# Optimization experiments

Measured on AMD Instinct MI355X. Metric: run time of the kernel, lower is better.

The kernel has to match this reference:

```python
import jax, jax.numpy as jnp
import numpy as np

NP_, NT_, NA_, NG_ = 50000, 200000, 20000, 500
ED, HID, H, C, L = 64, 64, 4, 16, 2
NEG_SLOPE = 0.2


def _edges(key, e, ns, nd):
    k1, k2 = jax.random.split(key)
    return jnp.stack([jax.random.randint(k1, (e,), 0, ns, dtype=jnp.int32),
                      jax.random.randint(k2, (e,), 0, nd, dtype=jnp.int32)])


def setup_inputs() -> dict:
    key = jax.random.key(0)
    ks = iter(jax.random.split(key, 64))
    nrm = lambda shp, s=0.1: (jax.random.normal(next(ks), shp, jnp.float32) * s)
    inp = {
        'playlist_x': nrm((NP_, 8), 1.0), 'track_x': nrm((NT_, 7), 1.0),
        'artist_x': nrm((NA_, 1), 1.0), 'genre_x': nrm((NG_, NG_), 1.0),
        'emb_playlist': nrm((NP_, ED)), 'emb_artist': nrm((NA_, ED)),
        'pf_W': nrm((8, ED)), 'pf_b': jnp.zeros((ED,)),
        'tf_W': nrm((7, ED)), 'tf_b': jnp.zeros((ED,)),
        'af_W': nrm((1, ED)), 'af_b': jnp.zeros((ED,)),
        'gf_W': nrm((NG_, ED)), 'gf_b': jnp.zeros((ED,)),
        'ip_W_playlist': nrm((2 * ED, HID)), 'ip_b_playlist': jnp.zeros((HID,)),
        'ip_W_track': nrm((ED, HID)), 'ip_b_track': jnp.zeros((HID,)),
        'ip_W_artist': nrm((2 * ED, HID)), 'ip_b_artist': jnp.zeros((HID,)),
        'ip_W_genre': nrm((ED, HID)), 'ip_b_genre': jnp.zeros((HID,)),
        # 8 relations x L layers, shared lin per relation (PyG GATConv with int in_channels)
        'gat_W': nrm((L, 8, HID, H * C)), 'gat_b': jnp.zeros((L, 8, H * C)),
        'gat_as': nrm((L, 8, H, C)), 'gat_ad': nrm((L, 8, H, C)),
        'ln_w': jnp.ones((L, HID)), 'ln_b': jnp.zeros((L, HID)),
        'op_W_playlist': nrm((HID, ED)), 'op_b_playlist': jnp.zeros((ED,)),
        'op_W_track': nrm((HID, ED)), 'op_b_track': jnp.zeros((ED,)),
        'op_W_artist': nrm((HID, ED)), 'op_b_artist': jnp.zeros((ED,)),
        'op_W_genre': nrm((HID, ED)), 'op_b_genre': jnp.zeros((ED,)),
        'playlist_idx': jnp.arange(NP_, dtype=jnp.int32),
        'artist_idx': jnp.arange(NA_, dtype=jnp.int32),
        'ei_contains': _edges(next(ks), 1000000, NP_, NT_),
        'ei_in_playlist': _edges(next(ks), 1000000, NT_, NP_),
        'ei_by': _edges(next(ks), 200000, NT_, NA_),
        'ei_created': _edges(next(ks), 200000, NA_, NT_),
        'ei_has_genre': _edges(next(ks), 600000, NT_, NG_),
        'ei_includes': _edges(next(ks), 600000, NG_, NT_),
        'ei_performs': _edges(next(ks), 60000, NA_, NG_),
        'ei_performed_by': _edges(next(ks), 60000, NG_, NA_),
    }
    return inp


def _gat(x_src, x_dst, ei, W, b, a_s, a_d, n_dst):
    # PyG GATConv: shared lin, edge softmax over dst, scatter-add aggregation
    hs = (x_src @ W).reshape(x_src.shape[0], H, C)
    hd = (x_dst @ W).reshape(x_dst.shape[0], H, C)
    es, ed = ei[0], ei[1]
    al_s = jnp.einsum('nhc,hc->nh', hs, a_s)  # [Ns,H]
    al_d = jnp.einsum('nhc,hc->nh', hd, a_d)  # [Nd,H]
    alpha = jax.nn.leaky_relu(al_s[es] + al_d[ed], NEG_SLOPE)  # [E,H]
    amax = jax.ops.segment_max(alpha, ed, num_segments=n_dst)
    amax = jnp.where(jnp.isfinite(amax), amax, 0.0)
    ex = jnp.exp(alpha - amax[ed])
    den = jax.ops.segment_sum(ex, ed, num_segments=n_dst)
    coef = ex / (den[ed] + 1e-16)
    msg = (hs[es] * coef[:, :, None]).reshape(es.shape[0], H * C)  # [E,H*C]
    return jax.ops.segment_sum(msg, ed, num_segments=n_dst) + b


def _ln(x, w, b):
    m = jnp.mean(x, -1, keepdims=True)
    v = jnp.mean((x - m) ** 2, -1, keepdims=True)
    return (x - m) * jax.lax.rsqrt(v + 1e-5) * w + b


def _forward(playlist_x, track_x, artist_x, genre_x, emb_playlist, emb_artist,
             pf_W, pf_b, tf_W, tf_b, af_W, af_b, gf_W, gf_b,
             ip_W_playlist, ip_b_playlist, ip_W_track, ip_b_track,
             ip_W_artist, ip_b_artist, ip_W_genre, ip_b_genre,
             gat_W, gat_b, gat_as, gat_ad, ln_w, ln_b,
             op_W_playlist, op_b_playlist, op_W_track, op_b_track,
             op_W_artist, op_b_artist, op_W_genre, op_b_genre,
             playlist_idx, artist_idx, ei_contains, ei_in_playlist, ei_by,
             ei_created, ei_has_genre, ei_includes, ei_performs, ei_performed_by):
    h_p = jnp.concatenate([emb_playlist[playlist_idx], playlist_x @ pf_W + pf_b], -1) @ ip_W_playlist + ip_b_playlist
    h_t = (track_x @ tf_W + tf_b) @ ip_W_track + ip_b_track
    h_a = jnp.concatenate([emb_artist[artist_idx], artist_x @ af_W + af_b], -1) @ ip_W_artist + ip_b_artist
    h_g = (genre_x @ gf_W + gf_b) @ ip_W_genre + ip_b_genre
    for i in range(L):
        pp, pt, pa, pg = h_p, h_t, h_a, h_g
        g = lambda r, xs, xd, ei, nd: _gat(xs, xd, ei, gat_W[i, r], gat_b[i, r], gat_as[i, r], gat_ad[i, r], nd)
        # relation index: 0 contains,1 in_playlist,2 by,3 created,4 has_genre,5 includes_track,6 performs_genre,7 performed_by
        nt = g(0, pp, pt, ei_contains, NT_) + g(3, pa, pt, ei_created, NT_) + g(5, pg, pt, ei_includes, NT_)
        np2 = g(1, pt, pp, ei_in_playlist, NP_)
        na = g(2, pt, pa, ei_by, NA_) + g(7, pg, pa, ei_performed_by, NA_)
        ng = g(4, pt, pg, ei_has_genre, NG_) + g(6, pa, pg, ei_performs, NG_)
        h_p, h_t, h_a, h_g = jax.nn.relu(np2), jax.nn.relu(nt), jax.nn.relu(na), jax.nn.relu(ng)
        if i > 0:  # residual only after first layer (matches `if i > 0`)
            h_p, h_t, h_a, h_g = h_p + pp, h_t + pt, h_a + pa, h_g + pg
        h_p, h_t, h_a, h_g = (_ln(v, ln_w[i], ln_b[i]) for v in (h_p, h_t, h_a, h_g))
    return jnp.concatenate([
        h_p @ op_W_playlist + op_b_playlist,
        h_t @ op_W_track + op_b_track,
        h_a @ op_W_artist + op_b_artist,
        h_g @ op_W_genre + op_b_genre], axis=0)  # [NP+NT+NA+NG, 64]


def reference(playlist_x, track_x, artist_x, genre_x, emb_playlist, emb_artist,
              pf_W, pf_b, tf_W, tf_b, af_W, af_b, gf_W, gf_b,
              ip_W_playlist, ip_b_playlist, ip_W_track, ip_b_track,
              ip_W_artist, ip_b_artist, ip_W_genre, ip_b_genre,
              gat_W, gat_b, gat_as, gat_ad, ln_w, ln_b,
              op_W_playlist, op_b_playlist, op_W_track, op_b_track,
              op_W_artist, op_b_artist, op_W_genre, op_b_genre,
              playlist_idx, artist_idx, ei_contains, ei_in_playlist, ei_by,
              ei_created, ei_has_genre, ei_includes, ei_performs, ei_performed_by):
    return _forward(playlist_x, track_x, artist_x, genre_x, emb_playlist, emb_artist,
                    pf_W, pf_b, tf_W, tf_b, af_W, af_b, gf_W, gf_b,
                    ip_W_playlist, ip_b_playlist, ip_W_track, ip_b_track,
                    ip_W_artist, ip_b_artist, ip_W_genre, ip_b_genre,
                    gat_W, gat_b, gat_as, gat_ad, ln_w, ln_b,
                    op_W_playlist, op_b_playlist, op_W_track, op_b_track,
                    op_W_artist, op_b_artist, op_W_genre, op_b_genre,
                    playlist_idx, artist_idx, ei_contains, ei_in_playlist, ei_by,
                    ei_created, ei_has_genre, ei_includes, ei_performs, ei_performed_by)
```

## Files before the change

kernel.cpp:

```cpp
#include <hip/hip_runtime.h>
#include <cstdint>

constexpr int NP=50000, NT=200000, NA=20000, NG=500;
constexpr int NTOT = NP+NT+NA+NG;
constexpr int RO_P=0, RO_T=NP, RO_A=NP+NT, RO_G=NP+NT+NA;
constexpr int E_TOT = 3720000;

constexpr int H_E [8] = {1000000,1000000,200000,200000,600000,600000,60000,60000};
constexpr int H_ES[9] = {0,1000000,2000000,2200000,2400000,3000000,3600000,3660000,3720000};
constexpr int H_NS[8] = {NP,NT,NT,NA,NT,NG,NA,NG};
constexpr int H_ND[8] = {NT,NP,NA,NT,NG,NT,NG,NA};
constexpr int H_SO[8] = {RO_P,RO_T,RO_T,RO_A,RO_T,RO_G,RO_A,RO_G};
constexpr int H_DO[8] = {RO_T,RO_P,RO_A,RO_T,RO_G,RO_T,RO_G,RO_A};
constexpr int H_RPO[8]= {0,200001,250002,270003,470004,470505,670506,671007};
constexpr int H_CO[8] = {0,200000,250000,270000,470000,470500,670500,671000};

__constant__ int c_E [8] = {1000000,1000000,200000,200000,600000,600000,60000,60000};
__constant__ int c_ES[9] = {0,1000000,2000000,2200000,2400000,3000000,3600000,3660000,3720000};
__constant__ int c_ND[8] = {200000,50000,20000,200000,500,200000,500,20000};
__constant__ int c_RPO[8]= {0,200001,250002,270003,470004,470505,670506,671007};
__constant__ int c_CO[8] = {0,200000,250000,270000,470000,470500,670500,671000};

__constant__ int sb_pref[9] = {0,196,245,265,461,462,658,659,679};
constexpr int SB_BLOCKS = 679;

constexpr int WSZ = 16384;
__constant__ int c_G [8] = {16,16,4,4,10,10,2,2};
__constant__ int c_CS[8] = {62500,62500,50000,50000,60000,60000,30000,30000};
__constant__ int c_NW[8] = {13,4,2,13,1,13,1,2};
__constant__ int gw_pref[9] = {0,208,272,280,332,342,472,474,478};
constexpr int GW_BLOCKS = 478;
__constant__ int c_C2[8] = {0,3200000,4000000,4080000,4880000,4885000,6885000,6886000};

constexpr int OWT=0;
constexpr int OBT=448;
constexpr int OWPX=512;
constexpr int OBP=1024;
constexpr int OAV=1088;
constexpr int OBA=1152;
constexpr int OBG=1216;
constexpr int OBAGG=1280;
constexpr int OWAS=1792;
constexpr int OWAD=5888;
constexpr int OWG=9984;

struct EiPtrs { const int* p[8]; };

__device__ __forceinline__ unsigned short f2bf(float f){
  unsigned u = __float_as_uint(f);
  u += 0x7FFF + ((u>>16)&1);
  return (unsigned short)(u>>16);
}
__device__ __forceinline__ float bf2f(unsigned short b){
  return __uint_as_float(((unsigned)b)<<16);
}

__global__ __launch_bounds__(256) void k_prep(
  const float* __restrict__ pf_W, const float* __restrict__ pf_b,
  const float* __restrict__ tf_W, const float* __restrict__ tf_b,
  const float* __restrict__ af_W, const float* __restrict__ af_b,
  const float* __restrict__ gf_W, const float* __restrict__ gf_b,
  const float* __restrict__ ipWp, const float* __restrict__ ipbp,
  const float* __restrict__ ipWt, const float* __restrict__ ipbt,
  const float* __restrict__ ipWa, const float* __restrict__ ipba,
  const float* __restrict__ ipWg, const float* __restrict__ ipbg,
  const float* __restrict__ gatW, const float* __restrict__ gatB,
  const float* __restrict__ gatAs, const float* __restrict__ gatAd,
  float* __restrict__ cb)
{
  int tid = blockIdx.x*256 + threadIdx.x;
  int STR = gridDim.x*256;
  for(int i=tid;i<7*64;i+=STR){ int j=i>>6,c=i&63; float s=0.f;
    for(int k=0;k<64;k++) s += tf_W[j*64+k]*ipWt[k*64+c];
    cb[OWT+i]=s; }
  for(int i=tid;i<64;i+=STR){ float s=ipbt[i];
    for(int k=0;k<64;k++) s += tf_b[k]*ipWt[k*64+i];
    cb[OBT+i]=s; }
  for(int i=tid;i<8*64;i+=STR){ int j=i>>6,c=i&63; float s=0.f;
    for(int k=0;k<64;k++) s += pf_W[j*64+k]*ipWp[(64+k)*64+c];
    cb[OWPX+i]=s; }
  for(int i=tid;i<64;i+=STR){ float s=ipbp[i];
    for(int k=0;k<64;k++) s += pf_b[k]*ipWp[(64+k)*64+i];
    cb[OBP+i]=s; }
  for(int i=tid;i<64;i+=STR){ float s=0.f;
    for(int k=0;k<64;k++) s += af_W[k]*ipWa[(64+k)*64+i];
    cb[OAV+i]=s; }
  for(int i=tid;i<64;i+=STR){ float s=ipba[i];
    for(int k=0;k<64;k++) s += af_b[k]*ipWa[(64+k)*64+i];
    cb[OBA+i]=s; }
  for(int i=tid;i<64;i+=STR){ float s=ipbg[i];
    for(int k=0;k<64;k++) s += gf_b[k]*ipWg[k*64+i];
    cb[OBG+i]=s; }
  for(int i=tid;i<512;i+=STR){ int l=i>>8, t=(i>>6)&3, c=i&63;
    const float* B = gatB + l*8*64; float s;
    if(t==0)      s = B[1*64+c];
    else if(t==1) s = B[0*64+c]+B[3*64+c]+B[5*64+c];
    else if(t==2) s = B[2*64+c]+B[7*64+c];
    else          s = B[4*64+c]+B[6*64+c];
    cb[OBAGG+i]=s; }
  for(int i=tid;i<2*8*64*4;i+=STR){ int h=i&3, k=(i>>2)&63, lr=i>>8;
    const float* as = gatAs + lr*64;
    cb[OWAS+i] = ((k>>4)==h) ? as[h*16 + (k&15)] : 0.f;
    const float* W  = gatW + (size_t)lr*4096;
    const float* ad = gatAd + lr*64 + h*16;
    float d=0.f;
    for(int c=0;c<16;c++){ d += W[k*64+h*16+c]*ad[c]; }
    cb[OWAD+i]=d; }
  for(int i=tid;i<512*64;i+=STR){ int g=i>>6,c=i&63; float s=0.f;
    if(g<500){ for(int k=0;k<64;k++) s += gf_W[g*64+k]*ipWg[k*64+c]; }
    cb[OWG+i]=s; }
}

#define MM_DECL  __shared__ float sX[64*65]; __shared__ float sW[64*68]; \
  int tid=threadIdx.x; int rt=(tid>>4)<<2, ct=(tid&15)<<2; float acc[4][4];

#define MM_LOOP() \
  _Pragma("unroll 8") \
  for(int k=0;k<64;k++){ \
    float4 wv = *(const float4*)&sW[k*68+ct]; \
    float x0=sX[(rt+0)*65+k], x1=sX[(rt+1)*65+k], x2=sX[(rt+2)*65+k], x3=sX[(rt+3)*65+k]; \
    acc[0][0]+=x0*wv.x; acc[0][1]+=x0*wv.y; acc[0][2]+=x0*wv.z; acc[0][3]+=x0*wv.w; \
    acc[1][0]+=x1*wv.x; acc[1][1]+=x1*wv.y; acc[1][2]+=x1*wv.z; acc[1][3]+=x1*wv.w; \
    acc[2][0]+=x2*wv.x; acc[2][1]+=x2*wv.y; acc[2][2]+=x2*wv.z; acc[2][3]+=x2*wv.w; \
    acc[3][0]+=x3*wv.x; acc[3][1]+=x3*wv.y; acc[3][2]+=x3*wv.z; acc[3][3]+=x3*wv.w; \
  }

template<bool ALS, bool B16>
__global__ __launch_bounds__(256) void k_mm64(const float* __restrict__ X, const float* __restrict__ W,
  const float* __restrict__ bias, float* __restrict__ Y, float* __restrict__ alsY,
  const float* __restrict__ was, int N)
{
  MM_DECL
  int row0 = blockIdx.x*64;
  for(int i=tid;i<4096;i+=256){
    int r=i>>6, k=i&63;
    sX[r*65+k] = (row0+r<N)? X[(size_t)(row0+r)*64+k] : 0.f;
    sW[r*68+k] = W[i];
  }
  __syncthreads();
  #pragma unroll
  for(int i=0;i<4;i++){ acc[i][0]=0.f;acc[i][1]=0.f;acc[i][2]=0.f;acc[i][3]=0.f; }
  MM_LOOP()
  float4 bv = make_float4(0.f,0.f,0.f,0.f);
  if(bias) bv = *(const float4*)&bias[ct];
  #pragma unroll
  for(int i=0;i<4;i++){
    int row=row0+rt+i;
    if(row<N){
      if(B16){
        ushort4 o;
        o.x=f2bf(acc[i][0]+bv.x); o.y=f2bf(acc[i][1]+bv.y);
        o.z=f2bf(acc[i][2]+bv.z); o.w=f2bf(acc[i][3]+bv.w);
        *(ushort4*)&((unsigned short*)Y)[(size_t)row*64+ct] = o;
      } else {
        *(float4*)&Y[(size_t)row*64+ct] =
          make_float4(acc[i][0]+bv.x, acc[i][1]+bv.y, acc[i][2]+bv.z, acc[i][3]+bv.w);
      }
    }
  }
  if(ALS){
    float4 w0 = *(const float4*)&was[(ct+0)*4];
    float4 w1 = *(const float4*)&was[(ct+1)*4];
    float4 w2 = *(const float4*)&was[(ct+2)*4];
    float4 w3 = *(const float4*)&was[(ct+3)*4];
    #pragma unroll
    for(int i=0;i<4;i++){
      float4 p;
      p.x = acc[i][0]*w0.x + acc[i][1]*w1.x + acc[i][2]*w2.x + acc[i][3]*w3.x;
      p.y = acc[i][0]*w0.y + acc[i][1]*w1.y + acc[i][2]*w2.y + acc[i][3]*w3.y;
      p.z = acc[i][0]*w0.z + acc[i][1]*w1.z + acc[i][2]*w2.z + acc[i][3]*w3.z;
      p.w = acc[i][0]*w0.w + acc[i][1]*w1.w + acc[i][2]*w2.w + acc[i][3]*w3.w;
      #pragma unroll
      for(int m=1;m<16;m<<=1){
        p.x+=__shfl_xor(p.x,m); p.y+=__shfl_xor(p.y,m);
        p.z+=__shfl_xor(p.z,m); p.w+=__shfl_xor(p.w,m);
      }
      int row=row0+rt+i;
      if((tid&15)==0 && row<N) *(float4*)&alsY[(size_t)row*4] = p;
    }
  }
}

constexpr int BP=(NP+63)/64, BT=(NT+63)/64, BA=(NA+63)/64;
__global__ __launch_bounds__(256) void k_init(
  const float* __restrict__ px, const float* __restrict__ tx, const float* __restrict__ ax,
  const float* __restrict__ embp, const float* __restrict__ emba,
  const int* __restrict__ pidx, const int* __restrict__ aidx,
  const float* __restrict__ ipWp, const float* __restrict__ ipWa,
  const float* __restrict__ cb, float* __restrict__ hout)
{
  MM_DECL
  __shared__ float sE[64*9];
  int bid = blockIdx.x;
  if(bid < BP){
    int row0 = bid*64;
    for(int i=tid;i<4096;i+=256){
      int r=i>>6,k=i&63; int row=row0+r;
      sX[r*65+k] = (row<NP)? embp[(size_t)pidx[row]*64+k] : 0.f;
      sW[r*68+k] = ipWp[i];
    }
    for(int i=tid;i<512;i+=256){ int r=i>>3,j=i&7; int row=row0+r;
      sE[r*9+j] = (row<NP)? px[(size_t)row*8+j] : 0.f; }
    __syncthreads();
    { float4 b = *(const float4*)&cb[OBP+ct];
      #pragma unroll
      for(int i=0;i<4;i++){ acc[i][0]=b.x;acc[i][1]=b.y;acc[i][2]=b.z;acc[i][3]=b.w; } }
    #pragma unroll
    for(int j=0;j<8;j++){
      float4 w = *(const float4*)&cb[OWPX + j*64 + ct];
      #pragma unroll
      for(int i=0;i<4;i++){ float xe = sE[(rt+i)*9+j];
        acc[i][0]+=xe*w.x; acc[i][1]+=xe*w.y; acc[i][2]+=xe*w.z; acc[i][3]+=xe*w.w; }
    }
    MM_LOOP()
    #pragma unroll
    for(int i=0;i<4;i++){ int row=row0+rt+i;
      if(row<NP) *(float4*)&hout[(size_t)(RO_P+row)*64+ct] =
        make_float4(acc[i][0],acc[i][1],acc[i][2],acc[i][3]); }
  } else if(bid < BP+BT){
    int row0 = (bid-BP)*64;
    for(int i=tid;i<512;i+=256){ int r=i>>3,j=i&7; int row=row0+r;
      sE[r*9+j] = (row<NT && j<7)? tx[(size_t)row*7+j] : 0.f; }
    __syncthreads();
    { float4 b = *(const float4*)&cb[OBT+ct];
      #pragma unroll
      for(int i=0;i<4;i++){ acc[i][0]=b.x;acc[i][1]=b.y;acc[i][2]=b.z;acc[i][3]=b.w; } }
    #pragma unroll
    for(int j=0;j<7;j++){
      float4 w = *(const float4*)&cb[OWT + j*64 + ct];
      #pragma unroll
      for(int i=0;i<4;i++){ float xe = sE[(rt+i)*9+j];
        acc[i][0]+=xe*w.x; acc[i][1]+=xe*w.y; acc[i][2]+=xe*w.z; acc[i][3]+=xe*w.w; }
    }
    #pragma unroll
    for(int i=0;i<4;i++){ int row=row0+rt+i;
      if(row<NT) *(float4*)&hout[(size_t)(RO_T+row)*64+ct] =
        make_float4(acc[i][0],acc[i][1],acc[i][2],acc[i][3]); }
  } else {
    int row0 = (bid-BP-BT)*64;
    for(int i=tid;i<4096;i+=256){
      int r=i>>6,k=i&63; int row=row0+r;
      sX[r*65+k] = (row<NA)? emba[(size_t)aidx[row]*64+k] : 0.f;
      sW[r*68+k] = ipWa[i];
    }
    for(int i=tid;i<64;i+=256){ int row=row0+i; sE[i] = (row<NA)? ax[row] : 0.f; }
    __syncthreads();
    #pragma unroll
    for(int i=0;i<4;i++){
      float4 b = *(const float4*)&cb[OBA+ct];
      float4 av = *(const float4*)&cb[OAV+ct];
      float xe = sE[rt+i];
      acc[i][0]=b.x+xe*av.x; acc[i][1]=b.y+xe*av.y; acc[i][2]=b.z+xe*av.z; acc[i][3]=b.w+xe*av.w;
    }
    MM_LOOP()
    #pragma unroll
    for(int i=0;i<4;i++){ int row=row0+rt+i;
      if(row<NA) *(float4*)&hout[(size_t)(RO_A+row)*64+ct] =
        make_float4(acc[i][0],acc[i][1],acc[i][2],acc[i][3]); }
  }
}

__global__ __launch_bounds__(256) void k_init_g(const float* __restrict__ gx,
  const float* __restrict__ cb, float* __restrict__ hout)
{
  int wid = (blockIdx.x<<2)|(threadIdx.x>>6);
  int lane = threadIdx.x&63;
  if(wid>=NG) return;
  float acc = cb[OBG+lane];
  const float* WG = cb+OWG;
  for(int kb=0;kb<512;kb+=64){
    int k = kb+lane;
    float xv = (k<500)? gx[(size_t)wid*500+k] : 0.f;
    for(int j=0;j<64;j++){
      float x = __shfl(xv, j);
      acc += x * WG[(size_t)(kb+j)*64+lane];
    }
  }
  hout[(size_t)(RO_G+wid)*64+lane] = acc;
}

__global__ __launch_bounds__(1024) void k_cnt2(EiPtrs ei, int* __restrict__ cnt2){
  __shared__ int wcnt[WSZ];
  int bid=blockIdx.x, tid=threadIdx.x;
  int r=0;
  #pragma unroll
  for(int q=1;q<8;q++) if(bid>=gw_pref[q]) r=q;
  int local = bid - gw_pref[r];
  int NW=c_NW[r];
  int g = local/NW, w = local-g*NW;
  int lo=w*WSZ, nd=c_ND[r], n=min(WSZ,nd-lo);
  for(int i=tid;i<n;i+=1024) wcnt[i]=0;
  __syncthreads();
  int E=c_E[r], CS=c_CS[r];
  int e0=g*CS, e1=min(e0+CS,E);
  const int* __restrict__ pd = ei.p[r]+E;
  for(int e=e0+tid;e<e1;e+=1024){
    int d = pd[e]-lo;
    if((unsigned)d < (unsigned)n) atomicAdd(&wcnt[d],1);
  }
  __syncthreads();
  int* c = cnt2 + c_C2[r] + g*nd + lo;
  for(int i=tid;i<n;i+=1024) c[i]=wcnt[i];
}

__global__ __launch_bounds__(1024) void k_scan1(const int* __restrict__ cnt2, int* __restrict__ bsum){
  int bid = blockIdx.x;
  int r=0;
  #pragma unroll
  for(int q=1;q<8;q++) if(bid>=sb_pref[q]) r=q;
  int lb = bid - sb_pref[r];
  int nd = c_ND[r];
  int idx = lb*1024 + threadIdx.x;
  int v = 0;
  if(idx<nd){
    int G=c_G[r]; int base=c_C2[r]+idx;
    for(int g=0;g<G;g++) v += cnt2[base+g*nd];
  }
  #pragma unroll
  for(int m=1;m<64;m<<=1) v += __shfl_xor(v,m);
  __shared__ int wsum[16];
  int lane = threadIdx.x&63, wid=threadIdx.x>>6;
  if(lane==0) wsum[wid]=v;
  __syncthreads();
  if(threadIdx.x==0){
    int s=0;
    #pragma unroll
    for(int w=0;w<16;w++) s+=wsum[w];
    bsum[bid]=s;
  }
}

__global__ __launch_bounds__(256) void k_scan2(int* __restrict__ bsum, int* __restrict__ rowptr){
  int r = blockIdx.x;
  int nb = sb_pref[r+1]-sb_pref[r];
  __shared__ int s[200];
  int tid=threadIdx.x;
  if(tid<nb) s[tid]=bsum[sb_pref[r]+tid];
  __syncthreads();
  if(tid==0){
    int run=0;
    for(int i=0;i<nb;i++){ int t=s[i]; s[i]=run; run+=t; }
    rowptr[c_RPO[r]+c_ND[r]] = run;
  }
  __syncthreads();
  if(tid<nb) bsum[sb_pref[r]+tid]=s[tid];
}

__global__ __launch_bounds__(1024) void k_scan3(const int* __restrict__ cnt2, const int* __restrict__ bsum,
  int* __restrict__ rowptr){
  int bid = blockIdx.x;
  int r=0;
  #pragma unroll
  for(int q=1;q<8;q++) if(bid>=sb_pref[q]) r=q;
  int lb = bid - sb_pref[r];
  int nd = c_ND[r];
  int tid = threadIdx.x;
  int idx = lb*1024 + tid;
  int v = 0;
  if(idx<nd){
    int G=c_G[r]; int base=c_C2[r]+idx;
    for(int g=0;g<G;g++) v += cnt2[base+g*nd];
  }
  __shared__ int s[1024];
  s[tid]=v;
  __syncthreads();
  #pragma unroll
  for(int off=1;off<1024;off<<=1){
    int t = (tid>=off)? s[tid-off] : 0;
    __syncthreads();
    s[tid]+=t;
    __syncthreads();
  }
  int ex = s[tid]-v + bsum[bid];
  if(idx<nd) rowptr[c_RPO[r]+idx]=ex;
}

__global__ __launch_bounds__(1024) void k_off2(const int* __restrict__ rowptr, int* __restrict__ cnt2){
  int bid = blockIdx.x;
  int r=0;
  #pragma unroll
  for(int q=1;q<8;q++) if(bid>=sb_pref[q]) r=q;
  int idx = (bid-sb_pref[r])*1024 + threadIdx.x;
  int nd = c_ND[r];
  if(idx<nd){
    int run = rowptr[c_RPO[r]+idx];
    int G=c_G[r]; int base=c_C2[r]+idx;
    for(int g=0;g<G;g++){
      int t = cnt2[base+g*nd];
      cnt2[base+g*nd] = run;
      run += t;
    }
  }
}

__global__ __launch_bounds__(1024) void k_scat2(EiPtrs ei, const int* __restrict__ off2,
  int* __restrict__ col){
  __shared__ int wcur[WSZ];
  int bid=blockIdx.x, tid=threadIdx.x;
  int r=0;
  #pragma unroll
  for(int q=1;q<8;q++) if(bid>=gw_pref[q]) r=q;
  int local = bid - gw_pref[r];
  int NW=c_NW[r];
  int g = local/NW, w = local-g*NW;
  int lo=w*WSZ, nd=c_ND[r], n=min(WSZ,nd-lo);
  const int* o = off2 + c_C2[r] + g*nd + lo;
  for(int i=tid;i<n;i+=1024) wcur[i]=o[i];
  __syncthreads();
  int E=c_E[r], CS=c_CS[r];
  int e0=g*CS, e1=min(e0+CS,E);
  const int* __restrict__ ps = ei.p[r];
  const int* __restrict__ pd = ps+E;
  int* cl = col + c_ES[r];
  for(int e=e0+tid;e<e1;e+=1024){
    int d = pd[e]-lo;
    if((unsigned)d < (unsigned)n){
      int pos = atomicAdd(&wcur[d],1);
      cl[pos] = ps[e];
    }
  }
}

template<bool FIRST>
__global__ __launch_bounds__(256) void k_agg(const int* __restrict__ rp, const int* __restrict__ col,
  const unsigned short* __restrict__ hs, const float* __restrict__ als,
  const float* __restrict__ Xd, const float* __restrict__ wad,
  float* __restrict__ out, int nd)
{
  int wid = (blockIdx.x<<2)|(threadIdx.x>>6);
  int lane = threadIdx.x&63;
  if(wid>=nd) return;
  float x = Xd[(size_t)wid*64+lane];
  float4 wv = *(const float4*)&wad[lane*4];
  float a0=x*wv.x, a1=x*wv.y, a2=x*wv.z, a3=x*wv.w;
  #pragma unroll
  for(int m=1;m<64;m<<=1){
    a0+=__shfl_xor(a0,m); a1+=__shfl_xor(a1,m); a2+=__shfl_xor(a2,m); a3+=__shfl_xor(a3,m);
  }
  int h = lane>>4;
  float adv = (h==0)?a0:(h==1)?a1:(h==2)?a2:a3;
  int start = rp[wid], end = rp[wid+1];
  float den=0.f, acc=0.f;
  int j = start;
  for(; j+4<=end; j+=4){
    int s0=col[j], s1=col[j+1], s2=col[j+2], s3=col[j+3];
    float A0=als[(size_t)s0*4+h], A1=als[(size_t)s1*4+h];
    float A2=als[(size_t)s2*4+h], A3=als[(size_t)s3*4+h];
    float h0=bf2f(hs[(size_t)s0*64+lane]), h1=bf2f(hs[(size_t)s1*64+lane]);
    float h2=bf2f(hs[(size_t)s2*64+lane]), h3=bf2f(hs[(size_t)s3*64+lane]);
    float v0=A0+adv; v0=fmaxf(v0,0.2f*v0); float e0=__expf(v0);
    float v1=A1+adv; v1=fmaxf(v1,0.2f*v1); float e1=__expf(v1);
    float v2=A2+adv; v2=fmaxf(v2,0.2f*v2); float e2=__expf(v2);
    float v3=A3+adv; v3=fmaxf(v3,0.2f*v3); float e3=__expf(v3);
    den+=e0; acc+=e0*h0;
    den+=e1; acc+=e1*h1;
    den+=e2; acc+=e2*h2;
    den+=e3; acc+=e3*h3;
  }
  for(; j<end; j++){
    int s = col[j];
    float ah = als[(size_t)s*4+h] + adv;
    ah = fmaxf(ah, 0.2f*ah);
    float e = __expf(ah);
    den += e;
    acc += e*bf2f(hs[(size_t)s*64+lane]);
  }
  float r = acc/(den+1e-16f);
  if(FIRST) out[(size_t)wid*64+lane] = r;
  else      out[(size_t)wid*64+lane] += r;
}

template<bool FIRST>
__global__ __launch_bounds__(1024) void k_agg_blk(const int* __restrict__ rp, const int* __restrict__ col,
  const unsigned short* __restrict__ hs, const float* __restrict__ als,
  const float* __restrict__ Xd, const float* __restrict__ wad,
  float* __restrict__ out, int nd)
{
  int d = blockIdx.x;
  if(d>=nd) return;
  int tid=threadIdx.x, lane=tid&63, wid=tid>>6;
  __shared__ float sden[16*4];
  __shared__ float sacc[16][64];
  float x = Xd[(size_t)d*64+lane];
  float4 wv = *(const float4*)&wad[lane*4];
  float a0=x*wv.x, a1=x*wv.y, a2=x*wv.z, a3=x*wv.w;
  #pragma unroll
  for(int m=1;m<64;m<<=1){
    a0+=__shfl_xor(a0,m); a1+=__shfl_xor(a1,m); a2+=__shfl_xor(a2,m); a3+=__shfl_xor(a3,m);
  }
  int h = lane>>4;
  float adv = (h==0)?a0:(h==1)?a1:(h==2)?a2:a3;
  int start = rp[d], end = rp[d+1];
  float den=0.f, acc=0.f;
  int j = start+wid;
  for(; j+48<end; j+=64){
    int s0=col[j], s1=col[j+16], s2=col[j+32], s3=col[j+48];
    float A0=als[(size_t)s0*4+h], A1=als[(size_t)s1*4+h];
    float A2=als[(size_t)s2*4+h], A3=als[(size_t)s3*4+h];
    float h0=bf2f(hs[(size_t)s0*64+lane]), h1=bf2f(hs[(size_t)s1*64+lane]);
    float h2=bf2f(hs[(size_t)s2*64+lane]), h3=bf2f(hs[(size_t)s3*64+lane]);
    float v0=A0+adv; v0=fmaxf(v0,0.2f*v0); float e0=__expf(v0);
    float v1=A1+adv; v1=fmaxf(v1,0.2f*v1); float e1=__expf(v1);
    float v2=A2+adv; v2=fmaxf(v2,0.2f*v2); float e2=__expf(v2);
    float v3=A3+adv; v3=fmaxf(v3,0.2f*v3); float e3=__expf(v3);
    den+=e0; acc+=e0*h0;
    den+=e1; acc+=e1*h1;
    den+=e2; acc+=e2*h2;
    den+=e3; acc+=e3*h3;
  }
  for(; j<end; j+=16){
    int s = col[j];
    float ah = als[(size_t)s*4+h] + adv;
    ah = fmaxf(ah, 0.2f*ah);
    float e = __expf(ah);
    den += e;
    acc += e*bf2f(hs[(size_t)s*64+lane]);
  }
  if((lane&15)==0) sden[wid*4+h]=den;
  sacc[wid][lane]=acc;
  __syncthreads();
  if(tid<64){
    float s=0.f, dt=0.f;
    #pragma unroll
    for(int w=0;w<16;w++){ s+=sacc[w][tid]; dt+=sden[w*4+(tid>>4)]; }
    float r = s/(dt+1e-16f);
    if(FIRST) out[(size_t)d*64+tid] = r;
    else      out[(size_t)d*64+tid] += r;
  }
}

__global__ __launch_bounds__(256) void k_post(float* __restrict__ hnew, const float* __restrict__ hold,
  const float* __restrict__ bagg, const float* __restrict__ lnw, const float* __restrict__ lnb, int layer)
{
  int wid = (blockIdx.x<<2)|(threadIdx.x>>6);
  int lane = threadIdx.x&63;
  if(wid>=NTOT) return;
  int t = (wid<RO_T)?0 : (wid<RO_A)?1 : (wid<RO_G)?2 : 3;
  size_t idx = (size_t)wid*64+lane;
  float v = hnew[idx] + bagg[t*64+lane];
  v = fmaxf(v, 0.f);
  if(layer) v += hold[idx];
  float s = v;
  #pragma unroll
  for(int m=1;m<64;m<<=1) s += __shfl_xor(s,m);
  float mu = s*(1.f/64.f);
  float d = v-mu;
  float q = d*d;
  #pragma unroll
  for(int m=1;m<64;m<<=1) q += __shfl_xor(q,m);
  float var = q*(1.f/64.f);
  hnew[idx] = d*rsqrtf(var+1e-5f)*lnw[lane] + lnb[lane];
}

extern "C" void kernel_launch(void* const* d_in, const int* in_sizes, int n_in,
                              void* d_out, int out_size, void* d_ws, size_t ws_size,
                              hipStream_t stream)
{
  const float* playlist_x=(const float*)d_in[0];
  const float* track_x   =(const float*)d_in[1];
  const float* artist_x  =(const float*)d_in[2];
  const float* genre_x   =(const float*)d_in[3];
  const float* embp=(const float*)d_in[4];
  const float* emba=(const float*)d_in[5];
  const float* pf_W=(const float*)d_in[6];  const float* pf_b=(const float*)d_in[7];
  const float* tf_W=(const float*)d_in[8];  const float* tf_b=(const float*)d_in[9];
  const float* af_W=(const float*)d_in[10]; const float* af_b=(const float*)d_in[11];
  const float* gf_W=(const float*)d_in[12]; const float* gf_b=(const float*)d_in[13];
  const float* ipWp=(const float*)d_in[14]; const float* ipbp=(const float*)d_in[15];
  const float* ipWt=(const float*)d_in[16]; const float* ipbt=(const float*)d_in[17];
  const float* ipWa=(const float*)d_in[18]; const float* ipba=(const float*)d_in[19];
  const float* ipWg=(const float*)d_in[20]; const float* ipbg=(const float*)d_in[21];
  const float* gatW=(const float*)d_in[22]; const float* gatB=(const float*)d_in[23];
  const float* gatAs=(const float*)d_in[24];const float* gatAd=(const float*)d_in[25];
  const float* lnw=(const float*)d_in[26];  const float* lnb=(const float*)d_in[27];
  const float* opWp=(const float*)d_in[28]; const float* opbp=(const float*)d_in[29];
  const float* opWt=(const float*)d_in[30]; const float* opbt=(const float*)d_in[31];
  const float* opWa=(const float*)d_in[32]; const float* opba=(const float*)d_in[33];
  const float* opWg=(const float*)d_in[34]; const float* opbg=(const float*)d_in[35];
  const int* pidx=(const int*)d_in[36];
  const int* aidx=(const int*)d_in[37];
  EiPtrs ei;
  for(int r=0;r<8;r++) ei.p[r]=(const int*)d_in[38+r];

  char* ws=(char*)d_ws;
  float* cb = (float*)ws;
  size_t o_hB  = 256*1024;
  float* hB = (float*)(ws+o_hB);
  size_t o_hs  = o_hB  + (size_t)NTOT*64*4;
  unsigned short* hs16 = (unsigned short*)(ws+o_hs);
  size_t o_als = o_hs  + (size_t)NT*64*2;
  float* als=(float*)(ws+o_als);
  size_t o_rp  = o_als + (size_t)NT*4*4;
  int* rowptr=(int*)(ws+o_rp);
  size_t o_col = o_rp  + 691008*4;
  int* col=(int*)(ws+o_col);
  int* cnt2=(int*)(ws+o_hs);
  int* bsum=cnt2+6926000;
  float* hA=(float*)d_out;

  k_prep<<<128,256,0,stream>>>(pf_W,pf_b,tf_W,tf_b,af_W,af_b,gf_W,gf_b,
      ipWp,ipbp,ipWt,ipbt,ipWa,ipba,ipWg,ipbg,gatW,gatB,gatAs,gatAd,cb);
  k_init<<<BP+BT+BA,256,0,stream>>>(playlist_x,track_x,artist_x,embp,emba,pidx,aidx,ipWp,ipWa,cb,hA);
  k_init_g<<<(NG+3)/4,256,0,stream>>>(genre_x,cb,hA);

  k_cnt2<<<GW_BLOCKS,1024,0,stream>>>(ei,cnt2);
  k_scan1<<<SB_BLOCKS,1024,0,stream>>>(cnt2,bsum);
  k_scan2<<<8,256,0,stream>>>(bsum,rowptr);
  k_scan3<<<SB_BLOCKS,1024,0,stream>>>(cnt2,bsum,rowptr);
  k_off2<<<SB_BLOCKS,1024,0,stream>>>(rowptr,cnt2);
  k_scat2<<<GW_BLOCKS,1024,0,stream>>>(ei,cnt2,col);

  for(int l=0;l<2;l++){
    float* hcur = l? hB : hA;
    float* hnew = l? hA : hB;
    for(int r=0;r<8;r++){
      int Ns=H_NS[r], Nd=H_ND[r];
      const float* Xs = hcur + (size_t)H_SO[r]*64;
      const float* Xd = hcur + (size_t)H_DO[r]*64;
      const float* W  = gatW + (size_t)(l*8+r)*4096;
      const float* was = cb+OWAS+(size_t)(l*8+r)*256;
      const float* wad = cb+OWAD+(size_t)(l*8+r)*256;
      float* outp = hnew + (size_t)H_DO[r]*64;
      bool first = (r==0)||(r==1)||(r==2)||(r==4);
      k_mm64<true,true><<<(Ns+63)/64,256,0,stream>>>(Xs,W,nullptr,(float*)hs16,als,was,Ns);
      if(r==4 || r==6){
        if(first) k_agg_blk<true ><<<Nd,1024,0,stream>>>(rowptr+H_RPO[r], col+H_ES[r], hs16, als, Xd, wad, outp, Nd);
        else      k_agg_blk<false><<<Nd,1024,0,stream>>>(rowptr+H_RPO[r], col+H_ES[r], hs16, als, Xd, wad, outp, Nd);
      } else {
        if(first) k_agg<true ><<<(Nd+3)/4,256,0,stream>>>(rowptr+H_RPO[r], col+H_ES[r], hs16, als, Xd, wad, outp, Nd);
        else      k_agg<false><<<(Nd+3)/4,256,0,stream>>>(rowptr+H_RPO[r], col+H_ES[r], hs16, als, Xd, wad, outp, Nd);
      }
    }
    k_post<<<(NTOT+3)/4,256,0,stream>>>(hnew, hcur, cb+OBAGG+l*256, lnw+l*64, lnb+l*64, l);
  }
  k_mm64<false,false><<<(NP+63)/64,256,0,stream>>>(hA+(size_t)RO_P*64, opWp, opbp, hA+(size_t)RO_P*64, nullptr, nullptr, NP);
  k_mm64<false,false><<<(NT+63)/64,256,0,stream>>>(hA+(size_t)RO_T*64, opWt, opbt, hA+(size_t)RO_T*64, nullptr, nullptr, NT);
  k_mm64<false,false><<<(NA+63)/64,256,0,stream>>>(hA+(size_t)RO_A*64, opWa, opba, hA+(size_t)RO_A*64, nullptr, nullptr, NA);
  k_mm64<false,false><<<(NG+63)/64,256,0,stream>>>(hA+(size_t)RO_G*64, opWg, opbg, hA+(size_t)RO_G*64, nullptr, nullptr, NG);
}
```

Before: 1.429 ms.

## Batch all relation projections and fuse per-destination GAT aggregation with layer norm

Replaces the per-relation loop of projection and aggregation launches with one batched projection kernel over all eight relations, writing into a combined workspace, and one per-node kernel. That kernel aggregates every incoming relation for a node, then applies bias, ReLU, residual and LayerNorm in place. This removes many kernel launches, the read-modify-write accumulation across relations, and the separate post pass. It needs a larger workspace and falls back to the old path when the workspace is too small. It also drops the block-per-node path for the genre relations, so each of the 500 genre nodes is handled by a single wavefront over thousands of edges, which risks a long tail.

```diff
diff --git a/kernel.cpp b/kernel.cpp
--- a/kernel.cpp
+++ b/kernel.cpp
@@ -20,6 +20,12 @@
 __constant__ int c_ND[8] = {200000,50000,20000,200000,500,200000,500,20000};
 __constant__ int c_RPO[8]= {0,200001,250002,270003,470004,470505,670506,671007};
 __constant__ int c_CO[8] = {0,200000,250000,270000,470000,470500,670500,671000};
+__constant__ int c_NS[8] = {50000,200000,200000,20000,200000,500,20000,500};
+__constant__ int c_SO[8] = {0,50000,50000,250000,50000,270000,250000,270000};
+__constant__ int c_DO[8] = {50000,0,250000,50000,270000,50000,270000,250000};
+__constant__ int c_RSO[8]= {0,50000,250000,450000,470000,670000,670500,690500};
+__constant__ int c_mmp[9]= {0,782,3907,7032,7345,10470,10478,10791,10799};
+constexpr int MM_ALL_BLOCKS = 10799;
 
 __constant__ int sb_pref[9] = {0,196,245,265,461,462,658,659,679};
 constexpr int SB_BLOCKS = 679;
@@ -181,6 +187,138 @@
   }
 }
 
+__global__ __launch_bounds__(256) void k_mm64_all(const float* __restrict__ hcur,
+  const float* __restrict__ gatW, const float* __restrict__ cb,
+  unsigned short* __restrict__ hs_all, float* __restrict__ als_all, int layer)
+{
+  MM_DECL
+  int bid = blockIdx.x;
+  int r=0;
+  #pragma unroll
+  for(int q=1;q<8;q++) if(bid>=c_mmp[q]) r=q;
+  int row0 = (bid - c_mmp[r])*64;
+  int N = c_NS[r];
+  const float* X = hcur + (size_t)c_SO[r]*64;
+  const float* W = gatW + (size_t)(layer*8+r)*4096;
+  const float* was = cb + OWAS + (size_t)(layer*8+r)*256;
+  unsigned short* Y = hs_all + (size_t)c_RSO[r]*64;
+  float* alsY = als_all + (size_t)c_RSO[r]*4;
+  for(int i=tid;i<4096;i+=256){
+    int rr=i>>6, k=i&63;
+    sX[rr*65+k] = (row0+rr<N)? X[(size_t)(row0+rr)*64+k] : 0.f;
+    sW[rr*68+k] = W[i];
+  }
+  __syncthreads();
+  #pragma unroll
+  for(int i=0;i<4;i++){ acc[i][0]=0.f;acc[i][1]=0.f;acc[i][2]=0.f;acc[i][3]=0.f; }
+  MM_LOOP()
+  #pragma unroll
+  for(int i=0;i<4;i++){
+    int row=row0+rt+i;
+    if(row<N){
+      ushort4 o;
+      o.x=f2bf(acc[i][0]); o.y=f2bf(acc[i][1]); o.z=f2bf(acc[i][2]); o.w=f2bf(acc[i][3]);
+      *(ushort4*)&Y[(size_t)row*64+ct] = o;
+    }
+  }
+  {
+    float4 w0 = *(const float4*)&was[(ct+0)*4];
+    float4 w1 = *(const float4*)&was[(ct+1)*4];
+    float4 w2 = *(const float4*)&was[(ct+2)*4];
+    float4 w3 = *(const float4*)&was[(ct+3)*4];
+    #pragma unroll
+    for(int i=0;i<4;i++){
+      float4 p;
+      p.x = acc[i][0]*w0.x + acc[i][1]*w1.x + acc[i][2]*w2.x + acc[i][3]*w3.x;
+      p.y = acc[i][0]*w0.y + acc[i][1]*w1.y + acc[i][2]*w2.y + acc[i][3]*w3.y;
+      p.z = acc[i][0]*w0.z + acc[i][1]*w1.z + acc[i][2]*w2.z + acc[i][3]*w3.z;
+      p.w = acc[i][0]*w0.w + acc[i][1]*w1.w + acc[i][2]*w2.w + acc[i][3]*w3.w;
+      #pragma unroll
+      for(int m=1;m<16;m<<=1){
+        p.x+=__shfl_xor(p.x,m); p.y+=__shfl_xor(p.y,m);
+        p.z+=__shfl_xor(p.z,m); p.w+=__shfl_xor(p.w,m);
+      }
+      int row=row0+rt+i;
+      if((tid&15)==0 && row<N) *(float4*)&alsY[(size_t)row*4] = p;
+    }
+  }
+}
+
+__global__ __launch_bounds__(256) void k_gat_all(const int* __restrict__ rowptr,
+  const int* __restrict__ col, const unsigned short* __restrict__ hs_all,
+  const float* __restrict__ als_all, const float* __restrict__ hcur,
+  float* __restrict__ hnew, const float* __restrict__ cb,
+  const float* __restrict__ lnw, const float* __restrict__ lnb, int layer)
+{
+  int n = (blockIdx.x<<2)|(threadIdx.x>>6);
+  int lane = threadIdx.x&63;
+  if(n>=NTOT) return;
+  int h = lane>>4;
+  float x = hcur[(size_t)n*64+lane];
+  int t, nr; int rl[3];
+  if(n<RO_T){ t=0; nr=1; rl[0]=1; rl[1]=0; rl[2]=0; }
+  else if(n<RO_A){ t=1; nr=3; rl[0]=0; rl[1]=3; rl[2]=5; }
+  else if(n<RO_G){ t=2; nr=2; rl[0]=2; rl[1]=7; rl[2]=0; }
+  else { t=3; nr=2; rl[0]=4; rl[1]=6; rl[2]=0; }
+  float res = 0.f;
+  for(int q=0;q<nr;q++){
+    int r = rl[q];
+    int dl = n - c_DO[r];
+    const float* wad = cb + OWAD + (size_t)(layer*8+r)*256;
+    float4 wv = *(const float4*)&wad[lane*4];
+    float a0=x*wv.x, a1=x*wv.y, a2=x*wv.z, a3=x*wv.w;
+    #pragma unroll
+    for(int m=1;m<64;m<<=1){
+      a0+=__shfl_xor(a0,m); a1+=__shfl_xor(a1,m); a2+=__shfl_xor(a2,m); a3+=__shfl_xor(a3,m);
+    }
+    float adv = (h==0)?a0:(h==1)?a1:(h==2)?a2:a3;
+    const int* rp = rowptr + c_RPO[r];
+    int start = rp[dl], end = rp[dl+1];
+    const int* cl = col + c_ES[r];
+    const unsigned short* hsr = hs_all + (size_t)c_RSO[r]*64;
+    const float* alsr = als_all + (size_t)c_RSO[r]*4;
+    float den=0.f, acc=0.f;
+    int j=start;
+    for(; j+4<=end; j+=4){
+      int s0=cl[j], s1=cl[j+1], s2=cl[j+2], s3=cl[j+3];
+      float A0=alsr[(size_t)s0*4+h], A1=alsr[(size_t)s1*4+h];
+      float A2=alsr[(size_t)s2*4+h], A3=alsr[(size_t)s3*4+h];
+      float h0=bf2f(hsr[(size_t)s0*64+lane]), h1=bf2f(hsr[(size_t)s1*64+lane]);
+      float h2=bf2f(hsr[(size_t)s2*64+lane]), h3=bf2f(hsr[(size_t)s3*64+lane]);
+      float v0=A0+adv; v0=fmaxf(v0,0.2f*v0); float e0=__expf(v0);
+      float v1=A1+adv; v1=fmaxf(v1,0.2f*v1); float e1=__expf(v1);
+      float v2=A2+adv; v2=fmaxf(v2,0.2f*v2); float e2=__expf(v2);
+      float v3=A3+adv; v3=fmaxf(v3,0.2f*v3); float e3=__expf(v3);
+      den+=e0; acc+=e0*h0;
+      den+=e1; acc+=e1*h1;
+      den+=e2; acc+=e2*h2;
+      den+=e3; acc+=e3*h3;
+    }
+    for(; j<end; j++){
+      int s = cl[j];
+      float ah = alsr[(size_t)s*4+h] + adv;
+      ah = fmaxf(ah, 0.2f*ah);
+      float e = __expf(ah);
+      den += e;
+      acc += e*bf2f(hsr[(size_t)s*64+lane]);
+    }
+    res += acc/(den+1e-16f);
+  }
+  float v = res + cb[OBAGG + layer*256 + t*64 + lane];
+  v = fmaxf(v, 0.f);
+  if(layer) v += x;
+  float s = v;
+  #pragma unroll
+  for(int m=1;m<64;m<<=1) s += __shfl_xor(s,m);
+  float mu = s*(1.f/64.f);
+  float d = v-mu;
+  float qd = d*d;
+  #pragma unroll
+  for(int m=1;m<64;m<<=1) qd += __shfl_xor(qd,m);
+  float var = qd*(1.f/64.f);
+  hnew[(size_t)n*64+lane] = d*rsqrtf(var+1e-5f)*lnw[lane] + lnb[lane];
+}
+
 constexpr int BP=(NP+63)/64, BT=(NT+63)/64, BA=(NA+63)/64;
 __global__ __launch_bounds__(256) void k_init(
   const float* __restrict__ px, const float* __restrict__ tx, const float* __restrict__ ax,
@@ -583,58 +721,100 @@
   for(int r=0;r<8;r++) ei.p[r]=(const int*)d_in[38+r];
 
   char* ws=(char*)d_ws;
+  float* hA=(float*)d_out;
   float* cb = (float*)ws;
+
   size_t o_hB  = 256*1024;
-  float* hB = (float*)(ws+o_hB);
-  size_t o_hs  = o_hB  + (size_t)NTOT*64*4;
-  unsigned short* hs16 = (unsigned short*)(ws+o_hs);
-  size_t o_als = o_hs  + (size_t)NT*64*2;
-  float* als=(float*)(ws+o_als);
-  size_t o_rp  = o_als + (size_t)NT*4*4;
-  int* rowptr=(int*)(ws+o_rp);
-  size_t o_col = o_rp  + 691008*4;
-  int* col=(int*)(ws+o_col);
-  int* cnt2=(int*)(ws+o_hs);
-  int* bsum=cnt2+6926000;
-  float* hA=(float*)d_out;
-
-  k_prep<<<128,256,0,stream>>>(pf_W,pf_b,tf_W,tf_b,af_W,af_b,gf_W,gf_b,
-      ipWp,ipbp,ipWt,ipbt,ipWa,ipba,ipWg,ipbg,gatW,gatB,gatAs,gatAd,cb);
-  k_init<<<BP+BT+BA,256,0,stream>>>(playlist_x,track_x,artist_x,embp,emba,pidx,aidx,ipWp,ipWa,cb,hA);
-  k_init_g<<<(NG+3)/4,256,0,stream>>>(genre_x,cb,hA);
-
-  k_cnt2<<<GW_BLOCKS,1024,0,stream>>>(ei,cnt2);
-  k_scan1<<<SB_BLOCKS,1024,0,stream>>>(cnt2,bsum);
-  k_scan2<<<8,256,0,stream>>>(bsum,rowptr);
-  k_scan3<<<SB_BLOCKS,1024,0,stream>>>(cnt2,bsum,rowptr);
-  k_off2<<<SB_BLOCKS,1024,0,stream>>>(rowptr,cnt2);
-  k_scat2<<<GW_BLOCKS,1024,0,stream>>>(ei,cnt2,col);
-
-  for(int l=0;l<2;l++){
-    float* hcur = l? hB : hA;
-    float* hnew = l? hA : hB;
-    for(int r=0;r<8;r++){
-      int Ns=H_NS[r], Nd=H_ND[r];
-      const float* Xs = hcur + (size_t)H_SO[r]*64;
-      const float* Xd = hcur + (size_t)H_DO[r]*64;
-      const float* W  = gatW + (size_t)(l*8+r)*4096;
-      const float* was = cb+OWAS+(size_t)(l*8+r)*256;
-      const float* wad = cb+OWAD+(size_t)(l*8+r)*256;
-      float* outp = hnew + (size_t)H_DO[r]*64;
-      bool first = (r==0)||(r==1)||(r==2)||(r==4);
-      k_mm64<true,true><<<(Ns+63)/64,256,0,stream>>>(Xs,W,nullptr,(float*)hs16,als,was,Ns);
-      if(r==4 || r==6){
-        if(first) k_agg_blk<true ><<<Nd,1024,0,stream>>>(rowptr+H_RPO[r], col+H_ES[r], hs16, als, Xd, wad, outp, Nd);
-        else      k_agg_blk<false><<<Nd,1024,0,stream>>>(rowptr+H_RPO[r], col+H_ES[r], hs16, als, Xd, wad, outp, Nd);
-      } else {
-        if(first) k_agg<true ><<<(Nd+3)/4,256,0,stream>>>(rowptr+H_RPO[r], col+H_ES[r], hs16, als, Xd, wad, outp, Nd);
-        else      k_agg<false><<<(Nd+3)/4,256,0,stream>>>(rowptr+H_RPO[r], col+H_ES[r], hs16, als, Xd, wad, outp, Nd);
+  size_t o_hs  = o_hB + (size_t)NTOT*64*4;
+  size_t B_hs   = (size_t)691000*64*2;
+  size_t o_als = o_hs + B_hs;
+  size_t B_als  = (size_t)691000*4*4;
+  size_t o_rp  = o_als + B_als;
+  size_t o_col = o_rp + 691008*4;
+  size_t NEED  = o_col + (size_t)E_TOT*4;
+
+  if(ws_size >= NEED){
+    float* hB = (float*)(ws+o_hB);
+    unsigned short* hs_all = (unsigned short*)(ws+o_hs);
+    float* als_all = (float*)(ws+o_als);
+    int* rowptr=(int*)(ws+o_rp);
+    int* col=(int*)(ws+o_col);
+    int* cnt2=(int*)(ws+o_hs);
+    int* bsum=cnt2+6926000;
+
+    k_prep<<<128,256,0,stream>>>(pf_W,pf_b,tf_W,tf_b,af_W,af_b,gf_W,gf_b,
+        ipWp,ipbp,ipWt,ipbt,ipWa,ipba,ipWg,ipbg,gatW,gatB,gatAs,gatAd,cb);
+    k_init<<<BP+BT+BA,256,0,stream>>>(playlist_x,track_x,artist_x,embp,emba,pidx,aidx,ipWp,ipWa,cb,hA);
+    k_init_g<<<(NG+3)/4,256,0,stream>>>(genre_x,cb,hA);
+
+    k_cnt2<<<GW_BLOCKS,1024,0,stream>>>(ei,cnt2);
+    k_scan1<<<SB_BLOCKS,1024,0,stream>>>(cnt2,bsum);
+    k_scan2<<<8,256,0,stream>>>(bsum,rowptr);
+    k_scan3<<<SB_BLOCKS,1024,0,stream>>>(cnt2,bsum,rowptr);
+    k_off2<<<SB_BLOCKS,1024,0,stream>>>(rowptr,cnt2);
+    k_scat2<<<GW_BLOCKS,1024,0,stream>>>(ei,cnt2,col);
+
+    for(int l=0;l<2;l++){
+      const float* hcur = l? hB : hA;
+      float* hnew = l? hA : hB;
+      k_mm64_all<<<MM_ALL_BLOCKS,256,0,stream>>>(hcur, gatW, cb, hs_all, als_all, l);
+      k_gat_all<<<(NTOT+3)/4,256,0,stream>>>(rowptr, col, hs_all, als_all, hcur, hnew, cb,
+          lnw+l*64, lnb+l*64, l);
+    }
+    k_mm64<false,false><<<(NP+63)/64,256,0,stream>>>(hA+(size_t)RO_P*64, opWp, opbp, hA+(size_t)RO_P*64, nullptr, nullptr, NP);
+    k_mm64<false,false><<<(NT+63)/64,256,0,stream>>>(hA+(size_t)RO_T*64, opWt, opbt, hA+(size_t)RO_T*64, nullptr, nullptr, NT);
+    k_mm64<false,false><<<(NA+63)/64,256,0,stream>>>(hA+(size_t)RO_A*64, opWa, opba, hA+(size_t)RO_A*64, nullptr, nullptr, NA);
+    k_mm64<false,false><<<(NG+63)/64,256,0,stream>>>(hA+(size_t)RO_G*64, opWg, opbg, hA+(size_t)RO_G*64, nullptr, nullptr, NG);
+  } else {
+    float* hB = (float*)(ws+o_hB);
+    unsigned short* hs16 = (unsigned short*)(ws+o_hs);
+    size_t f_als = o_hs + (size_t)NT*64*2;
+    float* als=(float*)(ws+f_als);
+    size_t f_rp  = f_als + (size_t)NT*4*4;
+    int* rowptr=(int*)(ws+f_rp);
+    size_t f_col = f_rp + 691008*4;
+    int* col=(int*)(ws+f_col);
+    int* cnt2=(int*)(ws+o_hs);
+    int* bsum=cnt2+6926000;
+
+    k_prep<<<128,256,0,stream>>>(pf_W,pf_b,tf_W,tf_b,af_W,af_b,gf_W,gf_b,
+        ipWp,ipbp,ipWt,ipbt,ipWa,ipba,ipWg,ipbg,gatW,gatB,gatAs,gatAd,cb);
+    k_init<<<BP+BT+BA,256,0,stream>>>(playlist_x,track_x,artist_x,embp,emba,pidx,aidx,ipWp,ipWa,cb,hA);
+    k_init_g<<<(NG+3)/4,256,0,stream>>>(genre_x,cb,hA);
+
+    k_cnt2<<<GW_BLOCKS,1024,0,stream>>>(ei,cnt2);
+    k_scan1<<<SB_BLOCKS,1024,0,stream>>>(cnt2,bsum);
+    k_scan2<<<8,256,0,stream>>>(bsum,rowptr);
+    k_scan3<<<SB_BLOCKS,1024,0,stream>>>(cnt2,bsum,rowptr);
+    k_off2<<<SB_BLOCKS,1024,0,stream>>>(rowptr,cnt2);
+    k_scat2<<<GW_BLOCKS,1024,0,stream>>>(ei,cnt2,col);
+
+    for(int l=0;l<2;l++){
+      float* hcur = l? hB : hA;
+      float* hnew = l? hA : hB;
+      for(int r=0;r<8;r++){
+        int Ns=H_NS[r], Nd=H_ND[r];
+        const float* Xs = hcur + (size_t)H_SO[r]*64;
+        const float* Xd = hcur + (size_t)H_DO[r]*64;
+        const float* W  = gatW + (size_t)(l*8+r)*4096;
+        const float* was = cb+OWAS+(size_t)(l*8+r)*256;
+        const float* wad = cb+OWAD+(size_t)(l*8+r)*256;
+        float* outp = hnew + (size_t)H_DO[r]*64;
+        bool first = (r==0)||(r==1)||(r==2)||(r==4);
+        k_mm64<true,true><<<(Ns+63)/64,256,0,stream>>>(Xs,W,nullptr,(float*)hs16,als,was,Ns);
+        if(r==4 || r==6){
+          if(first) k_agg_blk<true ><<<Nd,1024,0,stream>>>(rowptr+H_RPO[r], col+H_ES[r], hs16, als, Xd, wad, outp, Nd);
+          else      k_agg_blk<false><<<Nd,1024,0,stream>>>(rowptr+H_RPO[r], col+H_ES[r], hs16, als, Xd, wad, outp, Nd);
+        } else {
+          if(first) k_agg<true ><<<(Nd+3)/4,256,0,stream>>>(rowptr+H_RPO[r], col+H_ES[r], hs16, als, Xd, wad, outp, Nd);
+          else      k_agg<false><<<(Nd+3)/4,256,0,stream>>>(rowptr+H_RPO[r], col+H_ES[r], hs16, als, Xd, wad, outp, Nd);
+        }
       }
-    }
-    k_post<<<(NTOT+3)/4,256,0,stream>>>(hnew, hcur, cb+OBAGG+l*256, lnw+l*64, lnb+l*64, l);
-  }
-  k_mm64<false,false><<<(NP+63)/64,256,0,stream>>>(hA+(size_t)RO_P*64, opWp, opbp, hA+(size_t)RO_P*64, nullptr, nullptr, NP);
-  k_mm64<false,false><<<(NT+63)/64,256,0,stream>>>(hA+(size_t)RO_T*64, opWt, opbt, hA+(size_t)RO_T*64, nullptr, nullptr, NT);
-  k_mm64<false,false><<<(NA+63)/64,256,0,stream>>>(hA+(size_t)RO_A*64, opWa, opba, hA+(size_t)RO_A*64, nullptr, nullptr, NA);
-  k_mm64<false,false><<<(NG+63)/64,256,0,stream>>>(hA+(size_t)RO_G*64, opWg, opbg, hA+(size_t)RO_G*64, nullptr, nullptr, NG);
-}
+      k_post<<<(NTOT+3)/4,256,0,stream>>>(hnew, hcur, cb+OBAGG+l*256, lnw+l*64, lnb+l*64, l);
+    }
+    k_mm64<false,false><<<(NP+63)/64,256,0,stream>>>(hA+(size_t)RO_P*64, opWp, opbp, hA+(size_t)RO_P*64, nullptr, nullptr, NP);
+    k_mm64<false,false><<<(NT+63)/64,256,0,stream>>>(hA+(size_t)RO_T*64, opWt, opbt, hA+(size_t)RO_T*64, nullptr, nullptr, NT);
+    k_mm64<false,false><<<(NA+63)/64,256,0,stream>>>(hA+(size_t)RO_A*64, opWa, opba, hA+(size_t)RO_A*64, nullptr, nullptr, NA);
+    k_mm64<false,false><<<(NG+63)/64,256,0,stream>>>(hA+(size_t)RO_G*64, opWg, opbg, hA+(size_t)RO_G*64, nullptr, nullptr, NG);
+  }
+}
```

After: 1.655 ms. 1.16x slower.
